# Optimization experiments

Hardware: AMD Instinct MI355X
Metric: run time of the kernel (lower is better)

## Reference

```python
import jax, jax.numpy as jnp
import numpy as np

NUM_EXPERTS = 8
CAPACITY = 320  # per-batch per-expert token capacity


def setup_inputs() -> dict:
    key = jax.random.key(0)
    k0, k1, k2, k3 = jax.random.split(key, 4)
    B, S, D, F = 4, 2048, 1024, 4096
    E = NUM_EXPERTS
    hidden_states = jax.random.normal(k0, (B, S, D), dtype=jnp.float32)
    gate_w = jax.random.normal(k1, (E, D), dtype=jnp.float32) * 0.02
    w1 = jax.random.normal(k2, (E, D, F), dtype=jnp.float32) * 0.02
    w2 = jax.random.normal(k3, (E, F, D), dtype=jnp.float32) * 0.02
    return {"hidden_states": hidden_states, "gate_w": gate_w, "w1": w1, "w2": w2}


def reference(hidden_states, gate_w, w1, w2):
    E, C = NUM_EXPERTS, CAPACITY
    B, S, D = hidden_states.shape

    # --- route ---
    router_logits = jnp.einsum('bsd,ed->bse', hidden_states, gate_w)
    router_probs = jax.nn.softmax(router_logits, axis=-1)
    expert_idx = jnp.argmax(router_probs, axis=-1)                      # [B,S]
    onehot = jax.nn.one_hot(expert_idx, E, dtype=jnp.int32)             # [B,S,E]
    priority = jnp.cumsum(onehot, axis=1)                               # [B,S,E]
    router_mask = onehot * (priority <= C)                              # [B,S,E]
    assigned = jnp.sum(router_mask, axis=-1) > 0                        # [B,S]
    # slot within expert buffer; dropped tokens go to overflow slot C
    slot = jnp.where(assigned, jnp.sum(priority * onehot, axis=-1) - 1, C)  # [B,S]
    top_prob = jnp.max(router_probs, axis=-1, keepdims=True)            # [B,S,1]

    # --- dispatch: scatter tokens into [B,E,C+1,D] buffers ---
    def dispatch(x_b, e_b, s_b):
        return jnp.zeros((E, C + 1, D), x_b.dtype).at[e_b, s_b].set(x_b)
    buf = jax.vmap(dispatch)(hidden_states, expert_idx, slot)           # [B,E,C+1,D]

    # --- per-expert FFN as grouped GEMM ---
    h = jax.nn.silu(jnp.einsum('becd,edf->becf', buf, w1))
    y = jnp.einsum('becf,efd->becd', h, w2)                             # [B,E,C+1,D]

    # --- combine: gather expert outputs back to token order ---
    gathered = jax.vmap(lambda y_b, e_b, s_b: y_b[e_b, s_b])(y, expert_idx, slot)  # [B,S,D]
    next_states = jnp.where(assigned[..., None], gathered, hidden_states)
    out = top_prob * next_states

    # argmax of capacity-masked one-hot: dropped tokens -> expert 0
    expert_index = jnp.where(assigned, expert_idx, 0)
    return out, router_logits, expert_index
```

## Files before the change

### kernel.cpp

```cpp
#include <hip/hip_runtime.h>

#define B_  4
#define S_  2048
#define D_  1024
#define F_  4096
#define E_  8
#define C_  320
#define MPAD_ 1280
#define NT_ (B_*S_)

typedef short bf16x8 __attribute__((ext_vector_type(8)));
typedef float f32x4  __attribute__((ext_vector_type(4)));

using gptr_t = const __attribute__((address_space(1))) void*;
using lptr_t = __attribute__((address_space(3))) void*;

__device__ static inline void gll16(const void* g, void* l) {
    __builtin_amdgcn_global_load_lds((gptr_t)g, (lptr_t)l, 16, 0, 0);
}

__device__ static inline unsigned short f2b(float f) {
    unsigned int u = __float_as_uint(f);
    u += 0x7fffu + ((u >> 16) & 1u);
    return (unsigned short)(u >> 16);
}

__global__ __launch_bounds__(256) void k_convT(const float* __restrict__ in,
                                               unsigned short* __restrict__ out,
                                               int R, int Cc) {
    __shared__ unsigned short ld[64][66];
    int e = blockIdx.z;
    const float* src = in + (size_t)e * R * Cc;
    unsigned short* dst = out + (size_t)e * R * Cc;
    int c0 = blockIdx.x * 64, r0 = blockIdx.y * 64;
    int t = threadIdx.x;

    int rr = t >> 4;
    int cg = t & 15;
#pragma unroll
    for (int p = 0; p < 4; p++) {
        int row = p * 16 + rr;
        float4 v = *(const float4*)(src + (size_t)(r0 + row) * Cc + c0 + cg * 4);
        ld[cg * 4 + 0][row] = f2b(v.x);
        ld[cg * 4 + 1][row] = f2b(v.y);
        ld[cg * 4 + 2][row] = f2b(v.z);
        ld[cg * 4 + 3][row] = f2b(v.w);
    }
    __syncthreads();

    int cc = t >> 3;
    int rg = t & 7;
#pragma unroll
    for (int p = 0; p < 2; p++) {
        int col = p * 32 + cc;
        const unsigned* lp = (const unsigned*)&ld[col][rg * 8];
        uint4 w;
        w.x = lp[0]; w.y = lp[1]; w.z = lp[2]; w.w = lp[3];
        *(uint4*)(dst + (size_t)(c0 + col) * R + r0 + rg * 8) = w;
    }
}

__global__ __launch_bounds__(256) void k_router(const float* __restrict__ hs,
                                                const float* __restrict__ gw,
                                                float* __restrict__ logits,
                                                int* __restrict__ eidx,
                                                float* __restrict__ tp) {
    int tok  = (int)((blockIdx.x * 256 + threadIdx.x) >> 6);
    int lane = threadIdx.x & 63;
    const float* x = hs + (size_t)tok * D_;
    double acc[E_];
#pragma unroll
    for (int e = 0; e < E_; e++) acc[e] = 0.0;
    for (int i = 0; i < 16; i++) {
        float xv = x[lane + 64 * i];
#pragma unroll
        for (int e = 0; e < E_; e++)
            acc[e] += (double)xv * (double)gw[e * D_ + lane + 64 * i];
    }
#pragma unroll
    for (int e = 0; e < E_; e++) {
#pragma unroll
        for (int off = 32; off > 0; off >>= 1)
            acc[e] += __shfl_xor(acc[e], off, 64);
    }
    if (lane == 0) {
        float l[E_];
        float mx = -1e30f; int am = 0;
#pragma unroll
        for (int e = 0; e < E_; e++) {
            l[e] = (float)acc[e];
            if (l[e] > mx) { mx = l[e]; am = e; }
        }
        float se = 0.f;
#pragma unroll
        for (int e = 0; e < E_; e++) se += __expf(l[e] - mx);
        tp[tok]   = 1.0f / se;
        eidx[tok] = am;
#pragma unroll
        for (int e = 0; e < E_; e++) logits[(size_t)tok * E_ + e] = l[e];
    }
}

__global__ __launch_bounds__(256) void k_scan(const int* __restrict__ eidx,
                                              int* __restrict__ slot,
                                              int* __restrict__ tok_list,
                                              int* __restrict__ counts,
                                              float* __restrict__ eif) {
    int b = blockIdx.x;
    __shared__ int cCnt[32][E_];
    __shared__ int cBase[32][E_];
    int t = threadIdx.x, wv = t >> 6, lane = t & 63;
    const int* eb = eidx + b * S_;
    for (int c = wv; c < 32; c += 4) {
        int e = eb[c * 64 + lane];
#pragma unroll
        for (int x = 0; x < E_; x++) {
            unsigned long long m = __ballot(e == x);
            if (lane == 0) cCnt[c][x] = __popcll(m);
        }
    }
    __syncthreads();
    if (t < E_) {
        int s = 0;
        for (int c = 0; c < 32; c++) { cBase[c][t] = s; s += cCnt[c][t]; }
        counts[b * E_ + t] = s;
    }
    __syncthreads();
    for (int c = wv; c < 32; c += 4) {
        int s_tok = c * 64 + lane;
        int e = eb[s_tok];
        unsigned long long lowmask = (1ull << lane) - 1ull;
        int rank = 0;
#pragma unroll
        for (int x = 0; x < E_; x++) {
            unsigned long long m = __ballot(e == x);
            if (x == e) rank = __popcll(m & lowmask);
        }
        int pos = cBase[c][e] + rank;
        int assigned = (pos < C_);
        slot[b * S_ + s_tok] = assigned ? pos : C_;
        if (assigned) tok_list[(b * E_ + e) * C_ + pos] = s_tok;
        eif[b * S_ + s_tok] = assigned ? (float)e : 0.0f;
    }
}

__global__ void k_base(const int* __restrict__ counts,
                       int* __restrict__ ebase,
                       int* __restrict__ nE) {
    int e = threadIdx.x;
    if (e < E_) {
        int s = 0;
#pragma unroll
        for (int b = 0; b < B_; b++) {
            ebase[b * E_ + e] = s;
            s += min(counts[b * E_ + e], C_);
        }
        nE[e] = s;
    }
}

__global__ __launch_bounds__(256) void k_dispatch(const float* __restrict__ hs,
                                                  const int* __restrict__ tlB,
                                                  const int* __restrict__ ebase,
                                                  const int* __restrict__ nE,
                                                  int* __restrict__ tlG,
                                                  unsigned short* __restrict__ Xd) {
    int w    = (int)((blockIdx.x * 256 + threadIdx.x) >> 6);
    int lane = threadIdx.x & 63;
    int e = w / MPAD_, r = w - e * MPAD_;
    unsigned short* drow = Xd + ((size_t)e * MPAD_ + r) * D_;
    if (r < nE[e]) {
        int b = 0;
#pragma unroll
        for (int bb = 1; bb < B_; bb++) if (r >= ebase[bb * E_ + e]) b = bb;
        int pos = r - ebase[b * E_ + e];
        int ts  = tlB[(b * E_ + e) * C_ + pos];
        if (lane == 0) tlG[e * MPAD_ + r] = b * S_ + ts;
        const float* src = hs + ((size_t)b * S_ + ts) * D_;
#pragma unroll
        for (int i = 0; i < 2; i++) {
            int c0 = (lane + 64 * i) * 8;
            float4 v0 = *(const float4*)(src + c0);
            float4 v1 = *(const float4*)(src + c0 + 4);
            uint4 pk;
            pk.x = (unsigned)f2b(v0.x) | ((unsigned)f2b(v0.y) << 16);
            pk.y = (unsigned)f2b(v0.z) | ((unsigned)f2b(v0.w) << 16);
            pk.z = (unsigned)f2b(v1.x) | ((unsigned)f2b(v1.y) << 16);
            pk.w = (unsigned)f2b(v1.z) | ((unsigned)f2b(v1.w) << 16);
            *(uint4*)(drow + c0) = pk;
        }
    } else {
        uint4 zz = {0u, 0u, 0u, 0u};
#pragma unroll
        for (int i = 0; i < 2; i++)
            *(uint4*)(drow + (lane + 64 * i) * 8) = zz;
    }
}

template<int LDK, int KT>
__device__ __forceinline__ void gemm_core(const unsigned short* __restrict__ Ab,
                                          const unsigned short* __restrict__ Bb,
                                          char* sm, f32x4 (&acc)[8][4]) {
    const int t    = threadIdx.x;
    const int lane = t & 63;
    const int wv   = t >> 6;
    const int wm   = wv >> 2;
    const int wn   = wv & 3;

    const int sr = t >> 3;
    const int scs = (t & 7) ^ (sr & 7);
    const unsigned short* aS = Ab + (size_t)sr * LDK + scs * 8;
    const unsigned short* bS = Bb + (size_t)sr * LDK + scs * 8;
    char* ldsA = sm;
    char* ldsB = sm + 65536;
    const int sd = wv * 1024;

    const int rl  = lane & 15;
    const int sw  = lane & 7;
    const int kg  = lane >> 4;
    const int sx0 = ((kg    ) ^ sw) << 4;
    const int sx1 = ((kg + 4) ^ sw) << 4;
    const int aro = (wm * 128 + rl) * 128;
    const int bro = (wn * 64  + rl) * 128;

#pragma unroll
    for (int j = 0; j < 4; j++) {
        gll16(aS + (size_t)(j * 64) * LDK, ldsA + j * 8192 + sd);
        gll16(bS + (size_t)(j * 64) * LDK, ldsB + j * 8192 + sd);
    }
    asm volatile("s_waitcnt vmcnt(0)" ::: "memory");
    __builtin_amdgcn_sched_barrier(0);
    __builtin_amdgcn_s_barrier();
    __builtin_amdgcn_sched_barrier(0);

#pragma unroll 1
    for (int kt = 0; kt < KT; ++kt) {
        const char* cA = ldsA + (kt & 1) * 32768;
        const char* cB = ldsB + (kt & 1) * 32768;
        bf16x8 av[4], bv[4];

#pragma unroll
        for (int j = 0; j < 4; j++) bv[j] = *(const bf16x8*)(cB + bro + j * 2048 + sx0);
#pragma unroll
        for (int i = 0; i < 4; i++) av[i] = *(const bf16x8*)(cA + aro + i * 2048 + sx0);
        if (kt + 1 < KT) {
            char* nA = ldsA + ((kt + 1) & 1) * 32768;
            char* nB = ldsB + ((kt + 1) & 1) * 32768;
            const unsigned short* aP = aS + (kt + 1) * 64;
            const unsigned short* bP = bS + (kt + 1) * 64;
#pragma unroll
            for (int j = 0; j < 4; j++) {
                gll16(aP + (size_t)(j * 64) * LDK, nA + j * 8192 + sd);
                gll16(bP + (size_t)(j * 64) * LDK, nB + j * 8192 + sd);
            }
        }
        __builtin_amdgcn_sched_barrier(0);
        __builtin_amdgcn_s_barrier();
        __builtin_amdgcn_sched_barrier(0);
        __builtin_amdgcn_s_setprio(1);
#pragma unroll
        for (int i = 0; i < 4; i++)
#pragma unroll
            for (int j = 0; j < 4; j++)
                acc[i][j] = __builtin_amdgcn_mfma_f32_16x16x32_bf16(av[i], bv[j], acc[i][j], 0, 0, 0);
        __builtin_amdgcn_s_setprio(0);
        __builtin_amdgcn_sched_barrier(0);
        __builtin_amdgcn_s_barrier();
        __builtin_amdgcn_sched_barrier(0);

#pragma unroll
        for (int i = 0; i < 4; i++) av[i] = *(const bf16x8*)(cA + aro + 8192 + i * 2048 + sx0);
        __builtin_amdgcn_sched_barrier(0);
        __builtin_amdgcn_s_barrier();
        __builtin_amdgcn_sched_barrier(0);
        __builtin_amdgcn_s_setprio(1);
#pragma unroll
        for (int i = 0; i < 4; i++)
#pragma unroll
            for (int j = 0; j < 4; j++)
                acc[4 + i][j] = __builtin_amdgcn_mfma_f32_16x16x32_bf16(av[i], bv[j], acc[4 + i][j], 0, 0, 0);
        __builtin_amdgcn_s_setprio(0);
        __builtin_amdgcn_sched_barrier(0);
        __builtin_amdgcn_s_barrier();
        __builtin_amdgcn_sched_barrier(0);

#pragma unroll
        for (int j = 0; j < 4; j++) bv[j] = *(const bf16x8*)(cB + bro + j * 2048 + sx1);
#pragma unroll
        for (int i = 0; i < 4; i++) av[i] = *(const bf16x8*)(cA + aro + i * 2048 + sx1);
        __builtin_amdgcn_sched_barrier(0);
        __builtin_amdgcn_s_barrier();
        __builtin_amdgcn_sched_barrier(0);
        __builtin_amdgcn_s_setprio(1);
#pragma unroll
        for (int i = 0; i < 4; i++)
#pragma unroll
            for (int j = 0; j < 4; j++)
                acc[i][j] = __builtin_amdgcn_mfma_f32_16x16x32_bf16(av[i], bv[j], acc[i][j], 0, 0, 0);
        __builtin_amdgcn_s_setprio(0);
        __builtin_amdgcn_sched_barrier(0);
        __builtin_amdgcn_s_barrier();
        __builtin_amdgcn_sched_barrier(0);

#pragma unroll
        for (int i = 0; i < 4; i++) av[i] = *(const bf16x8*)(cA + aro + 8192 + i * 2048 + sx1);
        __builtin_amdgcn_sched_barrier(0);
        __builtin_amdgcn_s_barrier();
        __builtin_amdgcn_sched_barrier(0);
        __builtin_amdgcn_s_setprio(1);
#pragma unroll
        for (int i = 0; i < 4; i++)
#pragma unroll
            for (int j = 0; j < 4; j++)
                acc[4 + i][j] = __builtin_amdgcn_mfma_f32_16x16x32_bf16(av[i], bv[j], acc[4 + i][j], 0, 0, 0);
        __builtin_amdgcn_s_setprio(0);
        asm volatile("s_waitcnt vmcnt(0)" ::: "memory");
        __builtin_amdgcn_sched_barrier(0);
        __builtin_amdgcn_s_barrier();
        __builtin_amdgcn_sched_barrier(0);
    }
}

__global__ __launch_bounds__(512, 2) void k_ffn1(const unsigned short* __restrict__ Xd,
                                                 const unsigned short* __restrict__ w1t,
                                                 const int* __restrict__ nE,
                                                 unsigned short* __restrict__ h) {
    __shared__ __align__(16) char sm[131072];
    int id  = blockIdx.x;
    int e   = id & 7;
    int rem = id >> 3;
    int mt  = rem % 5;
    int nt  = rem / 5;
    int m0  = mt * 256;
    if (m0 >= nE[e]) return;
    int n0  = nt * 256;

    f32x4 acc[8][4];
    f32x4 z = {0.f, 0.f, 0.f, 0.f};
#pragma unroll
    for (int i = 0; i < 8; i++)
#pragma unroll
        for (int j = 0; j < 4; j++) acc[i][j] = z;

    const unsigned short* Ab = Xd  + ((size_t)e * MPAD_ + m0) * D_;
    const unsigned short* Bb = w1t + ((size_t)e * F_    + n0) * D_;
    gemm_core<D_, D_ / 64>(Ab, Bb, sm, acc);

    int lane = threadIdx.x & 63, wv = threadIdx.x >> 6, wm = wv >> 2, wn = wv & 3;
    unsigned short* hb = h + (size_t)e * MPAD_ * F_;
    int rb = m0 + wm * 128 + ((lane >> 4) << 2);
    int cb = n0 + wn * 64 + (lane & 15);
#pragma unroll
    for (int i = 0; i < 8; i++)
#pragma unroll
        for (int r = 0; r < 4; r++) {
            unsigned short* hr = hb + (size_t)(rb + i * 16 + r) * F_ + cb;
#pragma unroll
            for (int j = 0; j < 4; j++) {
                float v = acc[i][j][r];
                v = v / (1.0f + __expf(-v));
                hr[j * 16] = f2b(v);
            }
        }
}

__global__ __launch_bounds__(512, 2) void k_ffn2(const unsigned short* __restrict__ h,
                                                 const unsigned short* __restrict__ w2t,
                                                 const int* __restrict__ nE,
                                                 const int* __restrict__ tlG,
                                                 const float* __restrict__ tp,
                                                 float* __restrict__ out) {
    __shared__ __align__(16) char sm[131072];
    int id  = blockIdx.x;
    int e   = id & 7;
    int rem = id >> 3;
    int mt  = rem % 5;
    int nt  = rem / 5;
    int m0  = mt * 256;
    int n   = nE[e];
    if (m0 >= n) return;
    int n0  = nt * 256;

    f32x4 acc[8][4];
    f32x4 z = {0.f, 0.f, 0.f, 0.f};
#pragma unroll
    for (int i = 0; i < 8; i++)
#pragma unroll
        for (int j = 0; j < 4; j++) acc[i][j] = z;

    const unsigned short* Ab = h   + ((size_t)e * MPAD_ + m0) * F_;
    const unsigned short* Bb = w2t + ((size_t)e * D_    + n0) * F_;
    gemm_core<F_, F_ / 64>(Ab, Bb, sm, acc);

    int lane = threadIdx.x & 63, wv = threadIdx.x >> 6, wm = wv >> 2, wn = wv & 3;
    const int* tl = tlG + e * MPAD_;
    int rb = m0 + wm * 128 + ((lane >> 4) << 2);
    int cb = n0 + wn * 64 + (lane & 15);
#pragma unroll
    for (int i = 0; i < 8; i++)
#pragma unroll
        for (int r = 0; r < 4; r++) {
            int row = rb + i * 16 + r;
            if (row < n) {
                int gt = tl[row];
                float sc = tp[gt];
                float* orow = out + (size_t)gt * D_ + cb;
#pragma unroll
                for (int j = 0; j < 4; j++)
                    orow[j * 16] = sc * acc[i][j][r];
            }
        }
}

__global__ __launch_bounds__(256) void k_pass(const float* __restrict__ hs,
                                              const int* __restrict__ slot,
                                              const float* __restrict__ tp,
                                              float* __restrict__ out) {
    int tok  = (int)((blockIdx.x * 256 + threadIdx.x) >> 6);
    int lane = threadIdx.x & 63;
    if (slot[tok] < C_) return;
    float sc = tp[tok];
    const float* src = hs + (size_t)tok * D_;
    float* dst = out + (size_t)tok * D_;
#pragma unroll
    for (int i = 0; i < 4; i++) {
        float4 v = *(const float4*)(src + (lane + 64 * i) * 4);
        v.x *= sc; v.y *= sc; v.z *= sc; v.w *= sc;
        *(float4*)(dst + (lane + 64 * i) * 4) = v;
    }
}

extern "C" void kernel_launch(void* const* d_in, const int* in_sizes, int n_in,
                              void* d_out, int out_size, void* d_ws, size_t ws_size,
                              hipStream_t stream) {
    const float* hs = (const float*)d_in[0];
    const float* gw = (const float*)d_in[1];
    const float* w1 = (const float*)d_in[2];
    const float* w2 = (const float*)d_in[3];

    float* out    = (float*)d_out;
    float* logits = out + (size_t)NT_ * D_;
    float* eif    = logits + (size_t)NT_ * E_;

    char* ws = (char*)d_ws;
    int*            eidx   = (int*)(ws + 0);
    int*            slot   = (int*)(ws + 65536);
    float*          tp     = (float*)(ws + 131072);
    int*            tlB    = (int*)(ws + 196608);
    int*            tlG    = (int*)(ws + 237568);
    int*            counts = (int*)(ws + 278528);
    int*            ebase  = (int*)(ws + 278784);
    int*            nE     = (int*)(ws + 279040);
    unsigned short* Xd     = (unsigned short*)(ws + 327680);
    unsigned short* w1t    = (unsigned short*)(ws + 33554432ull);
    unsigned short* w2t    = (unsigned short*)(ws + 100663296ull);
    unsigned short* hbuf   = (unsigned short*)(ws + 167772160ull);

    dim3 blk(256);
    k_convT<<<dim3(F_ / 64, D_ / 64, E_), blk, 0, stream>>>(w1, w1t, D_, F_);
    k_convT<<<dim3(D_ / 64, F_ / 64, E_), blk, 0, stream>>>(w2, w2t, F_, D_);
    k_router<<<dim3(NT_ / 4), blk, 0, stream>>>(hs, gw, logits, eidx, tp);
    k_scan<<<dim3(B_), blk, 0, stream>>>(eidx, slot, tlB, counts, eif);
    k_base<<<dim3(1), dim3(64), 0, stream>>>(counts, ebase, nE);
    k_dispatch<<<dim3(E_ * MPAD_ / 4), blk, 0, stream>>>(hs, tlB, ebase, nE, tlG, Xd);
    k_ffn1<<<dim3(640), dim3(512), 0, stream>>>(Xd, w1t, nE, hbuf);
    k_ffn2<<<dim3(160), dim3(512), 0, stream>>>(hbuf, w2t, nE, tlG, tp, out);
    k_pass<<<dim3(NT_ / 4), blk, 0, stream>>>(hs, slot, tp, out);
}
```

Baseline: 610.3 us.

## Use 256x128 tiles with triple-buffered LDS prefetch two stages ahead in MoE GEMMs

The shared GEMM core drops from a 256x256 to a 256x128 output tile per block, with 8 waves arranged 4x2. The LDS ring grows from two to three slots so global-to-LDS loads run two k-steps ahead, with partial vmcnt waits in place of a full drain each iteration. Grid sizes double for both FFN kernels, which helps fill the machine, especially ffn2, which previously had only 160 blocks. In exchange, each block reuses less of B per tile and the per-step pipeline schedule becomes more intricate.

```diff
diff --git a/kernel.cpp b/kernel.cpp
--- a/kernel.cpp
+++ b/kernel.cpp
@@ -8,6 +8,7 @@
 #define C_  320
 #define MPAD_ 1280
 #define NT_ (B_*S_)
+#define SLOT_ 49152
 
 typedef short bf16x8 __attribute__((ext_vector_type(8)));
 typedef float f32x4  __attribute__((ext_vector_type(4)));
@@ -24,6 +25,10 @@
     u += 0x7fffu + ((u >> 16) & 1u);
     return (unsigned short)(u >> 16);
 }
+
+#define SB_() __builtin_amdgcn_sched_barrier(0)
+#define BAR_() do { SB_(); __builtin_amdgcn_s_barrier(); SB_(); } while (0)
+#define LGKM0_() do { asm volatile("s_waitcnt lgkmcnt(0)" ::: "memory"); SB_(); } while (0)
 
 __global__ __launch_bounds__(256) void k_convT(const float* __restrict__ in,
                                                unsigned short* __restrict__ out,
@@ -200,63 +205,61 @@
 template<int LDK, int KT>
 __device__ __forceinline__ void gemm_core(const unsigned short* __restrict__ Ab,
                                           const unsigned short* __restrict__ Bb,
-                                          char* sm, f32x4 (&acc)[8][4]) {
+                                          char* sm, f32x4 (&acc)[4][4]) {
     const int t    = threadIdx.x;
     const int lane = t & 63;
     const int wv   = t >> 6;
-    const int wm   = wv >> 2;
-    const int wn   = wv & 3;
-
-    const int sr = t >> 3;
+    const int wm   = wv >> 1;
+    const int wn   = wv & 1;
+
+    const int sr  = t >> 3;
     const int scs = (t & 7) ^ (sr & 7);
     const unsigned short* aS = Ab + (size_t)sr * LDK + scs * 8;
     const unsigned short* bS = Bb + (size_t)sr * LDK + scs * 8;
-    char* ldsA = sm;
-    char* ldsB = sm + 65536;
-    const int sd = wv * 1024;
+    const int wvoff = wv * 1024;
 
     const int rl  = lane & 15;
     const int sw  = lane & 7;
     const int kg  = lane >> 4;
     const int sx0 = ((kg    ) ^ sw) << 4;
     const int sx1 = ((kg + 4) ^ sw) << 4;
-    const int aro = (wm * 128 + rl) * 128;
-    const int bro = (wn * 64  + rl) * 128;
-
-#pragma unroll
-    for (int j = 0; j < 4; j++) {
-        gll16(aS + (size_t)(j * 64) * LDK, ldsA + j * 8192 + sd);
-        gll16(bS + (size_t)(j * 64) * LDK, ldsB + j * 8192 + sd);
-    }
-    asm volatile("s_waitcnt vmcnt(0)" ::: "memory");
-    __builtin_amdgcn_sched_barrier(0);
-    __builtin_amdgcn_s_barrier();
-    __builtin_amdgcn_sched_barrier(0);
-
+    const int aro = (wm * 64 + rl) * 128;
+    const int bro = (wn * 64 + rl) * 128;
+
+#pragma unroll
+    for (int g = 0; g < 2; g++) {
+        char* L = sm + g * SLOT_;
+        const unsigned short* aP = aS + (size_t)g * 64;
+        const unsigned short* bP = bS + (size_t)g * 64;
+#pragma unroll
+        for (int j = 0; j < 4; j++) gll16(aP + (size_t)j * 64 * LDK, L + j * 8192 + wvoff);
+#pragma unroll
+        for (int j = 0; j < 2; j++) gll16(bP + (size_t)j * 64 * LDK, L + 32768 + j * 8192 + wvoff);
+    }
+    asm volatile("s_waitcnt vmcnt(6)" ::: "memory");
+    BAR_();
+
+    int cslot = 0;
 #pragma unroll 1
     for (int kt = 0; kt < KT; ++kt) {
-        const char* cA = ldsA + (kt & 1) * 32768;
-        const char* cB = ldsB + (kt & 1) * 32768;
+        char* cs = sm + cslot * SLOT_;
+        const int ps = (cslot + 2 >= 3) ? cslot - 1 : cslot + 2;
+        char* L = sm + ps * SLOT_;
+        const unsigned short* aP = aS + (size_t)(kt + 2) * 64;
+        const unsigned short* bP = bS + (size_t)(kt + 2) * 64;
+        const bool pf = (kt + 2 < KT);
         bf16x8 av[4], bv[4];
 
 #pragma unroll
-        for (int j = 0; j < 4; j++) bv[j] = *(const bf16x8*)(cB + bro + j * 2048 + sx0);
-#pragma unroll
-        for (int i = 0; i < 4; i++) av[i] = *(const bf16x8*)(cA + aro + i * 2048 + sx0);
-        if (kt + 1 < KT) {
-            char* nA = ldsA + ((kt + 1) & 1) * 32768;
-            char* nB = ldsB + ((kt + 1) & 1) * 32768;
-            const unsigned short* aP = aS + (kt + 1) * 64;
-            const unsigned short* bP = bS + (kt + 1) * 64;
-#pragma unroll
-            for (int j = 0; j < 4; j++) {
-                gll16(aP + (size_t)(j * 64) * LDK, nA + j * 8192 + sd);
-                gll16(bP + (size_t)(j * 64) * LDK, nB + j * 8192 + sd);
-            }
-        }
-        __builtin_amdgcn_sched_barrier(0);
-        __builtin_amdgcn_s_barrier();
-        __builtin_amdgcn_sched_barrier(0);
+        for (int j = 0; j < 4; j++) bv[j] = *(const bf16x8*)(cs + 32768 + bro + j * 2048 + sx0);
+#pragma unroll
+        for (int i = 0; i < 4; i++) av[i] = *(const bf16x8*)(cs + aro + i * 2048 + sx0);
+        if (pf) {
+#pragma unroll
+            for (int j = 0; j < 3; j++) gll16(aP + (size_t)j * 64 * LDK, L + j * 8192 + wvoff);
+        }
+        BAR_();
+        LGKM0_();
         __builtin_amdgcn_s_setprio(1);
 #pragma unroll
         for (int i = 0; i < 4; i++)
@@ -264,33 +267,19 @@
             for (int j = 0; j < 4; j++)
                 acc[i][j] = __builtin_amdgcn_mfma_f32_16x16x32_bf16(av[i], bv[j], acc[i][j], 0, 0, 0);
         __builtin_amdgcn_s_setprio(0);
-        __builtin_amdgcn_sched_barrier(0);
-        __builtin_amdgcn_s_barrier();
-        __builtin_amdgcn_sched_barrier(0);
-
-#pragma unroll
-        for (int i = 0; i < 4; i++) av[i] = *(const bf16x8*)(cA + aro + 8192 + i * 2048 + sx0);
-        __builtin_amdgcn_sched_barrier(0);
-        __builtin_amdgcn_s_barrier();
-        __builtin_amdgcn_sched_barrier(0);
-        __builtin_amdgcn_s_setprio(1);
-#pragma unroll
-        for (int i = 0; i < 4; i++)
-#pragma unroll
-            for (int j = 0; j < 4; j++)
-                acc[4 + i][j] = __builtin_amdgcn_mfma_f32_16x16x32_bf16(av[i], bv[j], acc[4 + i][j], 0, 0, 0);
-        __builtin_amdgcn_s_setprio(0);
-        __builtin_amdgcn_sched_barrier(0);
-        __builtin_amdgcn_s_barrier();
-        __builtin_amdgcn_sched_barrier(0);
-
-#pragma unroll
-        for (int j = 0; j < 4; j++) bv[j] = *(const bf16x8*)(cB + bro + j * 2048 + sx1);
-#pragma unroll
-        for (int i = 0; i < 4; i++) av[i] = *(const bf16x8*)(cA + aro + i * 2048 + sx1);
-        __builtin_amdgcn_sched_barrier(0);
-        __builtin_amdgcn_s_barrier();
-        __builtin_amdgcn_sched_barrier(0);
+        BAR_();
+
+#pragma unroll
+        for (int j = 0; j < 4; j++) bv[j] = *(const bf16x8*)(cs + 32768 + bro + j * 2048 + sx1);
+#pragma unroll
+        for (int i = 0; i < 4; i++) av[i] = *(const bf16x8*)(cs + aro + i * 2048 + sx1);
+        if (pf) {
+            gll16(aP + (size_t)3 * 64 * LDK, L + 3 * 8192 + wvoff);
+#pragma unroll
+            for (int j = 0; j < 2; j++) gll16(bP + (size_t)j * 64 * LDK, L + 32768 + j * 8192 + wvoff);
+        }
+        BAR_();
+        LGKM0_();
         __builtin_amdgcn_s_setprio(1);
 #pragma unroll
         for (int i = 0; i < 4; i++)
@@ -298,26 +287,11 @@
             for (int j = 0; j < 4; j++)
                 acc[i][j] = __builtin_amdgcn_mfma_f32_16x16x32_bf16(av[i], bv[j], acc[i][j], 0, 0, 0);
         __builtin_amdgcn_s_setprio(0);
-        __builtin_amdgcn_sched_barrier(0);
-        __builtin_amdgcn_s_barrier();
-        __builtin_amdgcn_sched_barrier(0);
-
-#pragma unroll
-        for (int i = 0; i < 4; i++) av[i] = *(const bf16x8*)(cA + aro + 8192 + i * 2048 + sx1);
-        __builtin_amdgcn_sched_barrier(0);
-        __builtin_amdgcn_s_barrier();
-        __builtin_amdgcn_sched_barrier(0);
-        __builtin_amdgcn_s_setprio(1);
-#pragma unroll
-        for (int i = 0; i < 4; i++)
-#pragma unroll
-            for (int j = 0; j < 4; j++)
-                acc[4 + i][j] = __builtin_amdgcn_mfma_f32_16x16x32_bf16(av[i], bv[j], acc[4 + i][j], 0, 0, 0);
-        __builtin_amdgcn_s_setprio(0);
-        asm volatile("s_waitcnt vmcnt(0)" ::: "memory");
-        __builtin_amdgcn_sched_barrier(0);
-        __builtin_amdgcn_s_barrier();
-        __builtin_amdgcn_sched_barrier(0);
+        if (kt + 2 < KT)      { asm volatile("s_waitcnt vmcnt(6)" ::: "memory"); }
+        else if (kt + 1 < KT) { asm volatile("s_waitcnt vmcnt(0)" ::: "memory"); }
+        BAR_();
+
+        cslot = (cslot + 1 >= 3) ? 0 : cslot + 1;
     }
 }
 
@@ -325,7 +299,7 @@
                                                  const unsigned short* __restrict__ w1t,
                                                  const int* __restrict__ nE,
                                                  unsigned short* __restrict__ h) {
-    __shared__ __align__(16) char sm[131072];
+    __shared__ __align__(16) char sm[3 * SLOT_];
     int id  = blockIdx.x;
     int e   = id & 7;
     int rem = id >> 3;
@@ -333,12 +307,12 @@
     int nt  = rem / 5;
     int m0  = mt * 256;
     if (m0 >= nE[e]) return;
-    int n0  = nt * 256;
-
-    f32x4 acc[8][4];
+    int n0  = nt * 128;
+
+    f32x4 acc[4][4];
     f32x4 z = {0.f, 0.f, 0.f, 0.f};
 #pragma unroll
-    for (int i = 0; i < 8; i++)
+    for (int i = 0; i < 4; i++)
 #pragma unroll
         for (int j = 0; j < 4; j++) acc[i][j] = z;
 
@@ -346,12 +320,12 @@
     const unsigned short* Bb = w1t + ((size_t)e * F_    + n0) * D_;
     gemm_core<D_, D_ / 64>(Ab, Bb, sm, acc);
 
-    int lane = threadIdx.x & 63, wv = threadIdx.x >> 6, wm = wv >> 2, wn = wv & 3;
+    int lane = threadIdx.x & 63, wv = threadIdx.x >> 6, wm = wv >> 1, wn = wv & 1;
     unsigned short* hb = h + (size_t)e * MPAD_ * F_;
-    int rb = m0 + wm * 128 + ((lane >> 4) << 2);
+    int rb = m0 + wm * 64 + ((lane >> 4) << 2);
     int cb = n0 + wn * 64 + (lane & 15);
 #pragma unroll
-    for (int i = 0; i < 8; i++)
+    for (int i = 0; i < 4; i++)
 #pragma unroll
         for (int r = 0; r < 4; r++) {
             unsigned short* hr = hb + (size_t)(rb + i * 16 + r) * F_ + cb;
@@ -370,7 +344,7 @@
                                                  const int* __restrict__ tlG,
                                                  const float* __restrict__ tp,
                                                  float* __restrict__ out) {
-    __shared__ __align__(16) char sm[131072];
+    __shared__ __align__(16) char sm[3 * SLOT_];
     int id  = blockIdx.x;
     int e   = id & 7;
     int rem = id >> 3;
@@ -379,12 +353,12 @@
     int m0  = mt * 256;
     int n   = nE[e];
     if (m0 >= n) return;
-    int n0  = nt * 256;
-
-    f32x4 acc[8][4];
+    int n0  = nt * 128;
+
+    f32x4 acc[4][4];
     f32x4 z = {0.f, 0.f, 0.f, 0.f};
 #pragma unroll
-    for (int i = 0; i < 8; i++)
+    for (int i = 0; i < 4; i++)
 #pragma unroll
         for (int j = 0; j < 4; j++) acc[i][j] = z;
 
@@ -392,12 +366,12 @@
     const unsigned short* Bb = w2t + ((size_t)e * D_    + n0) * F_;
     gemm_core<F_, F_ / 64>(Ab, Bb, sm, acc);
 
-    int lane = threadIdx.x & 63, wv = threadIdx.x >> 6, wm = wv >> 2, wn = wv & 3;
+    int lane = threadIdx.x & 63, wv = threadIdx.x >> 6, wm = wv >> 1, wn = wv & 1;
     const int* tl = tlG + e * MPAD_;
-    int rb = m0 + wm * 128 + ((lane >> 4) << 2);
+    int rb = m0 + wm * 64 + ((lane >> 4) << 2);
     int cb = n0 + wn * 64 + (lane & 15);
 #pragma unroll
-    for (int i = 0; i < 8; i++)
+    for (int i = 0; i < 4; i++)
 #pragma unroll
         for (int r = 0; r < 4; r++) {
             int row = rb + i * 16 + r;
@@ -463,7 +437,7 @@
     k_scan<<<dim3(B_), blk, 0, stream>>>(eidx, slot, tlB, counts, eif);
     k_base<<<dim3(1), dim3(64), 0, stream>>>(counts, ebase, nE);
     k_dispatch<<<dim3(E_ * MPAD_ / 4), blk, 0, stream>>>(hs, tlB, ebase, nE, tlG, Xd);
-    k_ffn1<<<dim3(640), dim3(512), 0, stream>>>(Xd, w1t, nE, hbuf);
-    k_ffn2<<<dim3(160), dim3(512), 0, stream>>>(hbuf, w2t, nE, tlG, tp, out);
+    k_ffn1<<<dim3(1280), dim3(512), 0, stream>>>(Xd, w1t, nE, hbuf);
+    k_ffn2<<<dim3(320), dim3(512), 0, stream>>>(hbuf, w2t, nE, tlG, tp, out);
     k_pass<<<dim3(NT_ / 4), blk, 0, stream>>>(hs, slot, tp, out);
 }
```

Result: faster. 595.7 us (-2.4%).
